# Performance work log

Hardware: AMD Instinct MI355X
Metric: run time of the kernel (lower is better)

Reference implementation:

```python
import jax, jax.numpy as jnp
import numpy as np

H, D = 20, 64  # n_head, head_dim (n_state = 1280)


def setup_inputs() -> dict:
    key = jax.random.key(0)
    ks = jax.random.split(key, 14)
    B, S, N, R = 2, 1500, 1280, 32
    s = 0.05  # keep activations/scores numerically tame
    return {
        "x":   jax.random.normal(ks[0], (B, S, N), jnp.float32),
        "Wq1": jax.random.normal(ks[1], (R, N), jnp.float32) * s,
        "Wq2": jax.random.normal(ks[2], (N, R), jnp.float32) * s,
        "bq":  jax.random.normal(ks[3], (N,), jnp.float32) * s,
        "Wk1": jax.random.normal(ks[4], (R, N), jnp.float32) * s,
        "Wk2": jax.random.normal(ks[5], (N, R), jnp.float32) * s,
        "bk":  jax.random.normal(ks[6], (N,), jnp.float32) * s,
        "Wv1": jax.random.normal(ks[7], (R, N), jnp.float32) * s,
        "Wv2": jax.random.normal(ks[8], (N, R), jnp.float32) * s,
        "bv":  jax.random.normal(ks[9], (N,), jnp.float32) * s,
        "Wo1": jax.random.normal(ks[10], (R, N), jnp.float32) * s,
        "Wo2": jax.random.normal(ks[11], (N, R), jnp.float32) * s,
        "bo":  jax.random.normal(ks[12], (N,), jnp.float32) * s,
    }


def reference(x, Wq1, Wq2, bq, Wk1, Wk2, bk, Wv1, Wv2, bv, Wo1, Wo2, bo):
    B, S, N = x.shape
    # rank-r projections (the only full-size GEMMs over x)
    q1 = x @ Wq1.T  # (B,S,rq)
    k1 = x @ Wk1.T  # (B,S,rk)
    v1 = x @ Wv1.T  # (B,S,rv)
    # per-head factors, matching prepare_custom_kernel()
    Wq2h = Wq2.reshape(H, D, -1).transpose(0, 2, 1)  # (H,rq,D)
    Wk2h = Wk2.reshape(H, D, -1)                     # (H,D,rk)
    Wv2h = Wv2.reshape(H, D, -1).transpose(0, 2, 1)  # (H,rv,D)
    Wm = Wq2h @ Wk2h                                  # (H,rq,rk)
    bqh = bq.reshape(H, 1, D)                         # (H,1,D)
    bkh = bk.reshape(H, 1, D).transpose(0, 2, 1)      # (H,D,1)
    b1 = (Wq2h @ bkh)[:, :, 0]                        # (H,rq)
    b2 = (bqh @ Wk2h)[:, 0, :]                        # (H,rk)
    b3 = (bqh @ bkh)[:, 0, 0]                         # (H,)
    # merged low-rank attention scores: (q1 Wq2 + bq)(Wk2^T k1^T + bk)
    scores = jnp.einsum('bir,hrt,bjt->bhij', q1, Wm, k1)
    scores = scores + jnp.einsum('bir,hr->bhi', q1, b1)[:, :, :, None]
    scores = scores + jnp.einsum('bjt,ht->bhj', k1, b2)[:, :, None, :]
    scores = scores + b3[None, :, None, None]
    attn = jax.nn.softmax(scores * (D ** -0.5), axis=-1)  # SDPA default scale
    Vh = jnp.einsum('bjr,hrd->bhjd', v1, Wv2h)            # (B,H,S,D)
    a = jnp.einsum('bhij,bhjd->bhid', attn, Vh)           # (B,H,S,D)
    wv = a.transpose(0, 2, 1, 3).reshape(B, S, H * D) + bv
    # out projection (also low-rank)
    return (wv @ Wo1.T) @ Wo2.T + bo
```

## Files before the change

### kernel.cpp

```cpp
#include <hip/hip_runtime.h>
#include <math.h>

#define Bb 2
#define Ss 1500
#define SP 1536
#define Nn 1280
#define Hh 20
#define Rr 32
#define NT 24

typedef __attribute__((ext_vector_type(8))) short short8;
typedef __attribute__((ext_vector_type(4))) float f32x4;
typedef unsigned short ushort_t;

__device__ __forceinline__ unsigned short f2bf(float f) {
  unsigned u = __float_as_uint(f);
  u += 0x7fffu + ((u >> 16) & 1u);
  return (unsigned short)(u >> 16);
}
__device__ __forceinline__ float bf2f(unsigned short u) {
  return __uint_as_float((unsigned)u << 16);
}

__device__ __forceinline__ void gload16(const void* g, void* l) {
  __builtin_amdgcn_global_load_lds((const __attribute__((address_space(1))) unsigned int*)g,
                                   (__attribute__((address_space(3))) unsigned int*)l, 16, 0, 0);
}
__device__ __forceinline__ void gload4(const void* g, void* l) {
  __builtin_amdgcn_global_load_lds((const __attribute__((address_space(1))) unsigned int*)g,
                                   (__attribute__((address_space(3))) unsigned int*)l, 4, 0, 0);
}

#define BAR()                                  \
  do {                                         \
    asm volatile("" ::: "memory");             \
    __builtin_amdgcn_s_barrier();              \
    asm volatile("" ::: "memory");             \
  } while (0)

#define VMW(n) asm volatile("s_waitcnt vmcnt(" #n ")" ::: "memory")


__global__ void prep_kernel(const float* __restrict__ x, const float* __restrict__ Wq1,
                            const float* __restrict__ Wk1, const float* __restrict__ Wv1,
                            const float* __restrict__ Wo1, const float* __restrict__ Wq2,
                            const float* __restrict__ Wk2, const float* __restrict__ Wv2,
                            const float* __restrict__ bq, ushort_t* __restrict__ xb,
                            ushort_t* __restrict__ wcatb, ushort_t* __restrict__ wo1b,
                            ushort_t* __restrict__ wv2b, float* __restrict__ wm,
                            float* __restrict__ b2s) {
  int bid = blockIdx.x, tid = threadIdx.x;
  __shared__ float q2s[2048], k2s[2048], bqs[64];
  if (bid < 1920) {
    int gid = bid * 256 + tid;
    int gr = gid / 160, c8 = gid % 160;
    int b = gr / SP, i = gr - b * SP;
    short8 v = (short8){0, 0, 0, 0, 0, 0, 0, 0};
    if (i < Ss) {
      const float* src = x + ((size_t)(b * Ss + i)) * 1280 + c8 * 8;
      float4 a0 = *(const float4*)src;
      float4 a1 = *(const float4*)(src + 4);
      v[0] = (short)f2bf(a0.x); v[1] = (short)f2bf(a0.y);
      v[2] = (short)f2bf(a0.z); v[3] = (short)f2bf(a0.w);
      v[4] = (short)f2bf(a1.x); v[5] = (short)f2bf(a1.y);
      v[6] = (short)f2bf(a1.z); v[7] = (short)f2bf(a1.w);
    }
    *(short8*)(xb + (size_t)gr * 1280 + c8 * 8) = v;
  } else if (bid < 2060) {
    int gid = (bid - 1920) * 256 + tid;
    const float* src = nullptr;
    ushort_t* dst = nullptr;
    if (gid < 20480) {
      int row = gid / 160, c8 = gid % 160;
      dst = wcatb + (size_t)row * 1280 + c8 * 8;
      if (row < 32) src = Wq1 + (size_t)row * 1280 + c8 * 8;
      else if (row < 64) src = Wk1 + (size_t)(row - 32) * 1280 + c8 * 8;
      else if (row < 96) src = Wv1 + (size_t)(row - 64) * 1280 + c8 * 8;
    } else if (gid < 30720) {
      int g = gid - 20480;
      int row = g / 160, c8 = g % 160;
      dst = wo1b + (size_t)row * 1280 + c8 * 8;
      if (row < 32) src = Wo1 + (size_t)row * 1280 + c8 * 8;
    } else {
      int g = gid - 30720;
      int row = g >> 2, c8 = g & 3;
      dst = wv2b + row * 32 + c8 * 8;
      src = Wv2 + row * 32 + c8 * 8;
    }
    short8 v = (short8){0, 0, 0, 0, 0, 0, 0, 0};
    if (src) {
      #pragma unroll
      for (int j = 0; j < 8; ++j) v[j] = (short)f2bf(src[j]);
    }
    *(short8*)dst = v;
  } else {
    int h = bid - 2060;
    for (int e = tid; e < 2048; e += 256) {
      q2s[e] = Wq2[h * 2048 + e];
      k2s[e] = Wk2[h * 2048 + e];
    }
    if (tid < 64) bqs[tid] = bq[h * 64 + tid];
    __syncthreads();
    for (int e = tid; e < 1024; e += 256) {
      int r = e >> 5, t = e & 31;
      float s = 0.f;
      #pragma unroll 16
      for (int d = 0; d < 64; ++d) s += q2s[d * 32 + r] * k2s[d * 32 + t];
      wm[h * 1024 + r * 32 + t] = s * 0.125f;
    }
    if (tid < 32) {
      float s = 0.f;
      #pragma unroll 16
      for (int d = 0; d < 64; ++d) s += bqs[d] * k2s[d * 32 + tid];
      b2s[h * 32 + tid] = s * 0.125f;
    }
  }
}

__global__ __launch_bounds__(128) void gemm_qkv_kernel(
    const ushort_t* __restrict__ xbg, const ushort_t* __restrict__ wcat,
    float* __restrict__ xpq, ushort_t* __restrict__ k1b, ushort_t* __restrict__ v1b) {
  int tid = threadIdx.x, w = tid >> 6, l = tid & 63, l15 = l & 15, l4 = l >> 4;
  int row0 = blockIdx.x * 32;
  __shared__ __align__(16) short As[2][2048];
  __shared__ __align__(16) short Bs[2][6144];
  int sw8 = (((l & 7) ^ ((l >> 3) & 7)) << 3);
  const ushort_t* asrc0 = xbg + (size_t)(row0 + w * 16 + (l >> 3)) * 1280 + sw8;
  const ushort_t* asrc1 = asrc0 + (size_t)8 * 1280;
  const ushort_t* bsrc[6];
  #pragma unroll
  for (int g = 0; g < 6; ++g)
    bsrc[g] = wcat + (size_t)(w * 48 + g * 8 + (l >> 3)) * 1280 + sw8;

#define QSTAGE(bufi, kk)                                            \
  do {                                                              \
    gload16(asrc0 + (kk), &As[bufi][w * 1024]);                     \
    gload16(asrc1 + (kk), &As[bufi][w * 1024 + 512]);               \
    gload16(bsrc[0] + (kk), &Bs[bufi][w * 3072]);                   \
    gload16(bsrc[1] + (kk), &Bs[bufi][w * 3072 + 512]);             \
    gload16(bsrc[2] + (kk), &Bs[bufi][w * 3072 + 1024]);            \
    gload16(bsrc[3] + (kk), &Bs[bufi][w * 3072 + 1536]);            \
    gload16(bsrc[4] + (kk), &Bs[bufi][w * 3072 + 2048]);            \
    gload16(bsrc[5] + (kk), &Bs[bufi][w * 3072 + 2560]);            \
  } while (0)

  f32x4 acc[6];
  #pragma unroll
  for (int nf = 0; nf < 6; ++nf) acc[nf] = (f32x4){0.f, 0.f, 0.f, 0.f};

  QSTAGE(0, 0);
  int cur = 0;
  for (int t = 0; t < 20; ++t) {
    if (t < 19) {
      QSTAGE(cur ^ 1, (t + 1) * 64);
      VMW(8);
    } else {
      VMW(0);
    }
    BAR();
    #pragma unroll
    for (int ks = 0; ks < 2; ++ks) {
      short8 af = *(const short8*)&As[cur][(w * 16 + l15) * 64 +
                                           (((ks * 4 + l4) ^ (l15 & 7)) << 3)];
      #pragma unroll
      for (int nf = 0; nf < 6; ++nf) {
        short8 bf = *(const short8*)&Bs[cur][(nf * 16 + l15) * 64 +
                                             (((ks * 4 + l4) ^ (l15 & 7)) << 3)];
        acc[nf] = __builtin_amdgcn_mfma_f32_16x16x32_bf16(af, bf, acc[nf], 0, 0, 0);
      }
    }
    BAR();
    cur ^= 1;
  }
#undef QSTAGE

  #pragma unroll
  for (int nf = 0; nf < 6; ++nf) {
    int o = nf * 16 + l15;
    #pragma unroll
    for (int reg = 0; reg < 4; ++reg) {
      int gr = row0 + w * 16 + l4 * 4 + reg;
      int b = (gr >= SP) ? 1 : 0;
      int i = gr - b * SP;
      if (i < Ss) {
        float v = acc[nf][reg];
        if (o < 32) xpq[((size_t)b * Ss + i) * 32 + o] = v;
        else if (o < 64) k1b[((size_t)b * SP + i) * 32 + (o - 32)] = f2bf(v);
        else v1b[((size_t)b * 32 + (o - 64)) * SP + i] = f2bf(v);
      }
    }
  }
}

__global__ void qh_kb_kernel(const float* __restrict__ xpq, const float* __restrict__ wm,
                             const float* __restrict__ b2s, const ushort_t* __restrict__ k1b,
                             ushort_t* __restrict__ qhb, float* __restrict__ kbp) {
  int tid = threadIdx.x, b = blockIdx.z;
  if (blockIdx.y == 20) {
    int j0 = blockIdx.x * 64;
    __shared__ float k1s[64 * 33];
    __shared__ float b2sh[20 * 33];
    for (int e = tid; e < 2048; e += 256) {
      int row = e >> 5, t = e & 31;
      k1s[row * 33 + t] = bf2f(k1b[((size_t)b * SP + j0 + row) * 32 + t]);
    }
    for (int e = tid; e < 640; e += 256) b2sh[(e >> 5) * 33 + (e & 31)] = b2s[e];
    __syncthreads();
    for (int e = tid; e < 1280; e += 256) {
      int h = e >> 6, rw = e & 63;
      int j = j0 + rw;
      float s = -1e30f;
      if (j < Ss) {
        s = 0.f;
        #pragma unroll 8
        for (int t = 0; t < 32; ++t) s += k1s[rw * 33 + t] * b2sh[h * 33 + t];
      }
      kbp[((size_t)b * Hh + h) * SP + j] = s;
    }
  } else {
    int it = blockIdx.x, h = blockIdx.y;
    int i0 = it * 64;
    __shared__ float q1s[64 * 33];
    __shared__ float wms[1024];
    for (int e = tid; e < 2048; e += 256) {
      int row = e >> 5, r = e & 31;
      int i = i0 + row;
      q1s[row * 33 + r] = (i < Ss) ? xpq[((size_t)b * Ss + i) * 32 + r] : 0.f;
    }
    for (int e = tid; e < 1024; e += 256) wms[e] = wm[h * 1024 + e];
    __syncthreads();
    int row = tid >> 2, tc = (tid & 3) * 8;
    float o[8];
    #pragma unroll
    for (int j = 0; j < 8; ++j) o[j] = 0.f;
    for (int r = 0; r < 32; ++r) {
      float qv = q1s[row * 33 + r];
      #pragma unroll
      for (int j = 0; j < 8; ++j) o[j] += qv * wms[r * 32 + tc + j];
    }
    short8 sv;
    #pragma unroll
    for (int j = 0; j < 8; ++j) sv[j] = (short)f2bf(o[j]);
    *(short8*)(qhb + ((size_t)(b * Hh + h) * SP + i0 + row) * 32 + tc) = sv;
  }
}

__global__ __launch_bounds__(256) void attn2_kernel(
    const ushort_t* __restrict__ qhg, const ushort_t* __restrict__ k1g,
    const ushort_t* __restrict__ v1g, const ushort_t* __restrict__ wv2g,
    const float* __restrict__ kbg, const float* __restrict__ bv, ushort_t* __restrict__ wvb) {
  int it = blockIdx.x, h = blockIdx.y, b = blockIdx.z;
  int bh = b * Hh + h;
  int i0 = it * 64;
  int tid = threadIdx.x, w = tid >> 6, l = tid & 63;
  int l15 = l & 15, l4 = l >> 4;

  __shared__ short kS[2][2048];
  __shared__ short vS[2][2048];
  __shared__ float kbS[2][64];
  __shared__ short pS[4][1024];
  __shared__ short p2S[4][512];

  short8 qa = *(const short8*)(qhg + ((size_t)bh * SP + i0 + w * 16 + l15) * 32 + l4 * 8);
  short8 wb0 = *(const short8*)(wv2g + (size_t)(h * 64 + 0 * 16 + l15) * 32 + l4 * 8);
  short8 wb1 = *(const short8*)(wv2g + (size_t)(h * 64 + 1 * 16 + l15) * 32 + l4 * 8);
  short8 wb2 = *(const short8*)(wv2g + (size_t)(h * 64 + 2 * 16 + l15) * 32 + l4 * 8);
  short8 wb3 = *(const short8*)(wv2g + (size_t)(h * 64 + 3 * 16 + l15) * 32 + l4 * 8);
  VMW(0);

  const ushort_t* ksrc = k1g + (size_t)b * SP * 32 + l * 32 + w * 8;
  const ushort_t* vsrc =
      v1g + ((size_t)b * 32 + w * 8 + (l >> 3)) * SP + (((l & 7) ^ ((l >> 3) & 7)) << 3);
  const float* kbsrc = kbg + (size_t)bh * SP + l;

#define STAGE(bufi, tt)                                   \
  do {                                                    \
    int j0s = (tt) * 64;                                  \
    gload16(ksrc + (size_t)j0s * 32, &kS[bufi][w * 512]); \
    gload16(vsrc + j0s, &vS[bufi][w * 512]);              \
    if (w == 0) gload4(kbsrc + j0s, &kbS[bufi][0]);       \
  } while (0)

  STAGE(0, 0);

  f32x4 acc[4];
  #pragma unroll
  for (int db = 0; db < 4; ++db) acc[db] = (f32x4){0.f, 0.f, 0.f, 0.f};
  float psr[4] = {0.f, 0.f, 0.f, 0.f};
  const f32x4 zf = (f32x4){0.f, 0.f, 0.f, 0.f};

  int cur = 0;
  for (int t = 0; t < NT; ++t) {
    if (t < NT - 1) {
      STAGE(cur ^ 1, t + 1);
      if (w == 0) VMW(3); else VMW(2);
    } else {
      VMW(0);
    }
    BAR();

    #pragma unroll
    for (int nb = 0; nb < 4; ++nb) {
      short8 kf = *(const short8*)&kS[cur][l4 * 512 + (nb * 16 + l15) * 8];
      f32x4 c = __builtin_amdgcn_mfma_f32_16x16x32_bf16(qa, kf, zf, 0, 0, 0);
      float kbv = kbS[cur][nb * 16 + l15];
      int slot_lo = nb * 2 + (l15 >> 3);
      #pragma unroll
      for (int reg = 0; reg < 4; ++reg) {
        int q = l4 * 4 + reg;
        float p = __expf(c[reg] + kbv);
        unsigned short us = f2bf(p);
        psr[reg] += __uint_as_float((unsigned)us << 16);
        pS[w][q * 64 + ((slot_lo ^ (q & 7)) << 3) + (l15 & 7)] = (short)us;
      }
    }

    f32x4 pv1[2];
    pv1[0] = (f32x4){0.f, 0.f, 0.f, 0.f};
    pv1[1] = (f32x4){0.f, 0.f, 0.f, 0.f};
    #pragma unroll
    for (int kh = 0; kh < 2; ++kh) {
      short8 pa = *(const short8*)&pS[w][l15 * 64 + (((kh * 4 + l4) ^ (l15 & 7)) << 3)];
      #pragma unroll
      for (int nf = 0; nf < 2; ++nf) {
        short8 vf =
            *(const short8*)&vS[cur][(nf * 16 + l15) * 64 + (((kh * 4 + l4) ^ (l15 & 7)) << 3)];
        pv1[nf] = __builtin_amdgcn_mfma_f32_16x16x32_bf16(pa, vf, pv1[nf], 0, 0, 0);
      }
    }

    #pragma unroll
    for (int nf = 0; nf < 2; ++nf) {
      #pragma unroll
      for (int reg = 0; reg < 4; ++reg) {
        int q = l4 * 4 + reg;
        int slot = nf * 2 + (l15 >> 3);
        p2S[w][q * 32 + ((slot ^ ((q >> 1) & 3)) << 3) + (l15 & 7)] =
            (short)f2bf(pv1[nf][reg]);
      }
    }
    short8 pa2 = *(const short8*)&p2S[w][l15 * 32 + ((l4 ^ ((l15 >> 1) & 3)) << 3)];

    acc[0] = __builtin_amdgcn_mfma_f32_16x16x32_bf16(pa2, wb0, acc[0], 0, 0, 0);
    acc[1] = __builtin_amdgcn_mfma_f32_16x16x32_bf16(pa2, wb1, acc[1], 0, 0, 0);
    acc[2] = __builtin_amdgcn_mfma_f32_16x16x32_bf16(pa2, wb2, acc[2], 0, 0, 0);
    acc[3] = __builtin_amdgcn_mfma_f32_16x16x32_bf16(pa2, wb3, acc[3], 0, 0, 0);

    BAR();
    cur ^= 1;
  }
#undef STAGE

  #pragma unroll
  for (int reg = 0; reg < 4; ++reg) {
    #pragma unroll
    for (int m = 1; m < 16; m <<= 1) psr[reg] += __shfl_xor(psr[reg], m, 64);
  }
  float inv[4];
  #pragma unroll
  for (int reg = 0; reg < 4; ++reg) inv[reg] = 1.f / psr[reg];

  #pragma unroll
  for (int db = 0; db < 4; ++db) {
    float bvv = bv[h * 64 + db * 16 + l15];
    #pragma unroll
    for (int reg = 0; reg < 4; ++reg) {
      int qi = i0 + w * 16 + l4 * 4 + reg;
      if (qi < Ss)
        wvb[((size_t)(b * SP + qi)) * 1280 + h * 64 + db * 16 + l15] =
            f2bf(acc[db][reg] * inv[reg] + bvv);
    }
  }
}

__global__ __launch_bounds__(128) void gemm_o1_kernel(const ushort_t* __restrict__ wvg,
                                                      const ushort_t* __restrict__ wo1,
                                                      float* __restrict__ tbuf) {
  int tid = threadIdx.x, w = tid >> 6, l = tid & 63, l15 = l & 15, l4 = l >> 4;
  int row0 = blockIdx.x * 32;
  __shared__ __align__(16) short As[2][2048];
  __shared__ __align__(16) short Bs[2][2048];
  int sw8 = (((l & 7) ^ ((l >> 3) & 7)) << 3);
  const ushort_t* asrc0 = wvg + (size_t)(row0 + w * 16 + (l >> 3)) * 1280 + sw8;
  const ushort_t* asrc1 = asrc0 + (size_t)8 * 1280;
  const ushort_t* bsrc = wo1 + (size_t)(w * 16 + (l >> 3)) * 1280 + sw8;
  const ushort_t* bsrc1 = bsrc + (size_t)8 * 1280;

#define OSTAGE(bufi, kk)                                 \
  do {                                                   \
    gload16(asrc0 + (kk), &As[bufi][w * 1024]);          \
    gload16(asrc1 + (kk), &As[bufi][w * 1024 + 512]);    \
    gload16(bsrc + (kk), &Bs[bufi][w * 1024]);           \
    gload16(bsrc1 + (kk), &Bs[bufi][w * 1024 + 512]);    \
  } while (0)

  f32x4 acc[2];
  acc[0] = (f32x4){0.f, 0.f, 0.f, 0.f};
  acc[1] = (f32x4){0.f, 0.f, 0.f, 0.f};
  OSTAGE(0, 0);
  int cur = 0;
  for (int t = 0; t < 20; ++t) {
    if (t < 19) {
      OSTAGE(cur ^ 1, (t + 1) * 64);
      VMW(4);
    } else {
      VMW(0);
    }
    BAR();
    #pragma unroll
    for (int ks = 0; ks < 2; ++ks) {
      short8 af = *(const short8*)&As[cur][(w * 16 + l15) * 64 +
                                           (((ks * 4 + l4) ^ (l15 & 7)) << 3)];
      #pragma unroll
      for (int nf = 0; nf < 2; ++nf) {
        short8 bf = *(const short8*)&Bs[cur][(nf * 16 + l15) * 64 +
                                             (((ks * 4 + l4) ^ (l15 & 7)) << 3)];
        acc[nf] = __builtin_amdgcn_mfma_f32_16x16x32_bf16(af, bf, acc[nf], 0, 0, 0);
      }
    }
    BAR();
    cur ^= 1;
  }
#undef OSTAGE

  #pragma unroll
  for (int nf = 0; nf < 2; ++nf) {
    int o = nf * 16 + l15;
    #pragma unroll
    for (int reg = 0; reg < 4; ++reg) {
      int gr = row0 + w * 16 + l4 * 4 + reg;
      int b = (gr >= SP) ? 1 : 0;
      int i = gr - b * SP;
      if (i < Ss) tbuf[((size_t)b * Ss + i) * 32 + o] = acc[nf][reg];
    }
  }
}

__global__ void proj_o2_kernel(const float* __restrict__ tbuf, const float* __restrict__ Wo2,
                               const float* __restrict__ bo, float* __restrict__ out) {
  int rb = blockIdx.x, nb = blockIdx.y, tid = threadIdx.x;
  int rowbase = rb * 16, n0 = nb * 256;
  __shared__ float ts[16 * 33];
  __shared__ float wos[256 * 33];
  for (int e = tid; e < 8192; e += 256) {
    int nloc = e >> 5, o = e & 31;
    wos[nloc * 33 + o] = Wo2[(size_t)(n0 + nloc) * 32 + o];
  }
  for (int e = tid; e < 512; e += 256) {
    int row = e >> 5, o = e & 31;
    int gr = rowbase + row;
    ts[row * 33 + o] = (gr < Bb * Ss) ? tbuf[(size_t)gr * 32 + o] : 0.f;
  }
  __syncthreads();
  int n = n0 + tid;
  float bias = bo[n];
  for (int row = 0; row < 16; ++row) {
    int gr = rowbase + row;
    if (gr >= Bb * Ss) break;
    float s = bias;
    #pragma unroll 8
    for (int o = 0; o < 32; ++o) s += ts[row * 33 + o] * wos[tid * 33 + o];
    out[(size_t)gr * 1280 + n] = s;
  }
}

extern "C" void kernel_launch(void* const* d_in, const int* in_sizes, int n_in,
                              void* d_out, int out_size, void* d_ws, size_t ws_size,
                              hipStream_t stream) {
  const float* x   = (const float*)d_in[0];
  const float* Wq1 = (const float*)d_in[1];
  const float* Wq2 = (const float*)d_in[2];
  const float* bq  = (const float*)d_in[3];
  const float* Wk1 = (const float*)d_in[4];
  const float* Wk2 = (const float*)d_in[5];
  const float* Wv1 = (const float*)d_in[7];
  const float* Wv2 = (const float*)d_in[8];
  const float* bv  = (const float*)d_in[9];
  const float* Wo1 = (const float*)d_in[10];
  const float* Wo2 = (const float*)d_in[11];
  const float* bo  = (const float*)d_in[12];
  float* out = (float*)d_out;
  float* ws  = (float*)d_ws;

  if (ws_size < (size_t)5431424 * sizeof(float)) return;

  float* wm    = ws;
  float* b2s   = ws + 20480;
  float* xpq   = ws + 21120;
  float* kb    = ws + 117120;
  float* tbuf  = ws + 178560;
  ushort_t* qhb   = (ushort_t*)(ws + 274560);
  ushort_t* k1b   = (ushort_t*)(ws + 1257600);
  ushort_t* v1b   = (ushort_t*)(ws + 1306752);
  ushort_t* xb    = (ushort_t*)(ws + 1355904);
  ushort_t* wcatb = (ushort_t*)(ws + 3321984);
  ushort_t* wo1b  = (ushort_t*)(ws + 3403904);
  ushort_t* wv2b  = (ushort_t*)(ws + 3444864);
  ushort_t* wvb   = (ushort_t*)(ws + 3465344);

  prep_kernel<<<2080, 256, 0, stream>>>(x, Wq1, Wk1, Wv1, Wo1, Wq2, Wk2, Wv2, bq,
                                        xb, wcatb, wo1b, wv2b, wm, b2s);
  gemm_qkv_kernel<<<96, 128, 0, stream>>>(xb, wcatb, xpq, k1b, v1b);
  qh_kb_kernel<<<dim3(NT, 21, Bb), 256, 0, stream>>>(xpq, wm, b2s, k1b, qhb, kb);
  attn2_kernel<<<dim3(NT, Hh, Bb), 256, 0, stream>>>(qhb, k1b, v1b, wv2b, kb, bv, wvb);
  gemm_o1_kernel<<<96, 128, 0, stream>>>(wvb, wo1b, tbuf);
  proj_o2_kernel<<<dim3(188, 5), 256, 0, stream>>>(tbuf, Wo2, bo, out);
}
```

Measured before the change: 116.9 us.

## Accumulate P·V1 in rank space across tiles and apply Wv2 once after loop

The attention kernel now keeps the rank-32 P·V1 accumulator across all key tiles and projects through the per-head Wv2 factor once at the end, instead of rounding to bf16 and running four MFMAs per tile. The softmax exponent folds log2(e) into the precomputed score weights so it can use the raw v_exp_f32 instruction, and the bf16 packing uses v_cvt_pk_bf16_f32 instead of manual rounding. This removes per-tile LDS round trips, conversions and MFMAs from the inner loop. The row sum now accumulates unrounded fp32 probabilities while P·V uses the bf16-rounded values, a slight numerical mismatch.

Result: faster. 104.2 us (-10.9%).

```diff
diff --git a/kernel.cpp b/kernel.cpp
--- a/kernel.cpp
+++ b/kernel.cpp
@@ -9,6 +9,8 @@
 #define Rr 32
 #define NT 24
 
+#define LOG2E 1.44269504088896f
+
 typedef __attribute__((ext_vector_type(8))) short short8;
 typedef __attribute__((ext_vector_type(4))) float f32x4;
 typedef unsigned short ushort_t;
@@ -20,6 +22,16 @@
 }
 __device__ __forceinline__ float bf2f(unsigned short u) {
   return __uint_as_float((unsigned)u << 16);
+}
+__device__ __forceinline__ unsigned cvtpk(float a, float b) {
+  unsigned d;
+  asm("v_cvt_pk_bf16_f32 %0, %1, %2" : "=v"(d) : "v"(a), "v"(b));
+  return d;
+}
+__device__ __forceinline__ float fexp2(float x) {
+  float r;
+  asm("v_exp_f32 %0, %1" : "=v"(r) : "v"(x));
+  return r;
 }
 
 __device__ __forceinline__ void gload16(const void* g, void* l) {
@@ -106,13 +118,13 @@
       float s = 0.f;
       #pragma unroll 16
       for (int d = 0; d < 64; ++d) s += q2s[d * 32 + r] * k2s[d * 32 + t];
-      wm[h * 1024 + r * 32 + t] = s * 0.125f;
+      wm[h * 1024 + r * 32 + t] = s * (0.125f * LOG2E);
     }
     if (tid < 32) {
       float s = 0.f;
       #pragma unroll 16
       for (int d = 0; d < 64; ++d) s += bqs[d] * k2s[d * 32 + tid];
-      b2s[h * 32 + tid] = s * 0.125f;
+      b2s[h * 32 + tid] = s * (0.125f * LOG2E);
     }
   }
 }
@@ -283,9 +295,9 @@
 
   STAGE(0, 0);
 
-  f32x4 acc[4];
-  #pragma unroll
-  for (int db = 0; db < 4; ++db) acc[db] = (f32x4){0.f, 0.f, 0.f, 0.f};
+  f32x4 pv1[2];
+  pv1[0] = (f32x4){0.f, 0.f, 0.f, 0.f};
+  pv1[1] = (f32x4){0.f, 0.f, 0.f, 0.f};
   float psr[4] = {0.f, 0.f, 0.f, 0.f};
   const f32x4 zf = (f32x4){0.f, 0.f, 0.f, 0.f};
 
@@ -308,16 +320,12 @@
       #pragma unroll
       for (int reg = 0; reg < 4; ++reg) {
         int q = l4 * 4 + reg;
-        float p = __expf(c[reg] + kbv);
-        unsigned short us = f2bf(p);
-        psr[reg] += __uint_as_float((unsigned)us << 16);
-        pS[w][q * 64 + ((slot_lo ^ (q & 7)) << 3) + (l15 & 7)] = (short)us;
+        float p = fexp2(c[reg] + kbv);
+        psr[reg] += p;
+        pS[w][q * 64 + ((slot_lo ^ (q & 7)) << 3) + (l15 & 7)] = (short)cvtpk(p, p);
       }
     }
 
-    f32x4 pv1[2];
-    pv1[0] = (f32x4){0.f, 0.f, 0.f, 0.f};
-    pv1[1] = (f32x4){0.f, 0.f, 0.f, 0.f};
     #pragma unroll
     for (int kh = 0; kh < 2; ++kh) {
       short8 pa = *(const short8*)&pS[w][l15 * 64 + (((kh * 4 + l4) ^ (l15 & 7)) << 3)];
@@ -329,27 +337,28 @@
       }
     }
 
-    #pragma unroll
-    for (int nf = 0; nf < 2; ++nf) {
-      #pragma unroll
-      for (int reg = 0; reg < 4; ++reg) {
-        int q = l4 * 4 + reg;
-        int slot = nf * 2 + (l15 >> 3);
-        p2S[w][q * 32 + ((slot ^ ((q >> 1) & 3)) << 3) + (l15 & 7)] =
-            (short)f2bf(pv1[nf][reg]);
-      }
-    }
-    short8 pa2 = *(const short8*)&p2S[w][l15 * 32 + ((l4 ^ ((l15 >> 1) & 3)) << 3)];
-
-    acc[0] = __builtin_amdgcn_mfma_f32_16x16x32_bf16(pa2, wb0, acc[0], 0, 0, 0);
-    acc[1] = __builtin_amdgcn_mfma_f32_16x16x32_bf16(pa2, wb1, acc[1], 0, 0, 0);
-    acc[2] = __builtin_amdgcn_mfma_f32_16x16x32_bf16(pa2, wb2, acc[2], 0, 0, 0);
-    acc[3] = __builtin_amdgcn_mfma_f32_16x16x32_bf16(pa2, wb3, acc[3], 0, 0, 0);
-
     BAR();
     cur ^= 1;
   }
 #undef STAGE
+
+  #pragma unroll
+  for (int nf = 0; nf < 2; ++nf) {
+    #pragma unroll
+    for (int reg = 0; reg < 4; ++reg) {
+      int q = l4 * 4 + reg;
+      int slot = nf * 2 + (l15 >> 3);
+      p2S[w][q * 32 + ((slot ^ ((q >> 1) & 3)) << 3) + (l15 & 7)] =
+          (short)cvtpk(pv1[nf][reg], pv1[nf][reg]);
+    }
+  }
+  short8 pa2 = *(const short8*)&p2S[w][l15 * 32 + ((l4 ^ ((l15 >> 1) & 3)) << 3)];
+
+  f32x4 acc[4];
+  acc[0] = __builtin_amdgcn_mfma_f32_16x16x32_bf16(pa2, wb0, zf, 0, 0, 0);
+  acc[1] = __builtin_amdgcn_mfma_f32_16x16x32_bf16(pa2, wb1, zf, 0, 0, 0);
+  acc[2] = __builtin_amdgcn_mfma_f32_16x16x32_bf16(pa2, wb2, zf, 0, 0, 0);
+  acc[3] = __builtin_amdgcn_mfma_f32_16x16x32_bf16(pa2, wb3, zf, 0, 0, 0);
 
   #pragma unroll
   for (int reg = 0; reg < 4; ++reg) {
```
